# Kernel optimization log

Measured on AMD Instinct MI355X. Metric: run time of the kernel, lower is better.

## Reference

```python
import jax, jax.numpy as jnp
import numpy as np
from jax.ops import segment_sum

N_NODES = 100000
N_EDGES = 1600000
N_GRAPHS = 128


def setup_inputs() -> dict:
    key = jax.random.key(0)
    ks = jax.random.split(key, 16)
    x = jax.random.normal(ks[0], (N_NODES, 128), dtype=jnp.float32)
    edge_index = jax.random.randint(ks[1], (2, N_EDGES), 0, N_NODES, dtype=jnp.int64)
    batch = jnp.sort(jax.random.randint(ks[2], (N_NODES,), 0, N_GRAPHS, dtype=jnp.int64))
    def glorot(k, fan_in, fan_out):
        lim = (6.0 / (fan_in + fan_out)) ** 0.5
        return jax.random.uniform(k, (fan_in, fan_out), jnp.float32, -lim, lim)
    return {
        "x": x, "edge_index": edge_index, "batch": batch,
        "W1": glorot(ks[3], 128, 64), "b1": jnp.zeros((64,), jnp.float32),
        "W2": glorot(ks[4], 64, 64),  "b2": jnp.zeros((64,), jnp.float32),
        "W3": glorot(ks[5], 64, 64),  "b3": jnp.zeros((64,), jnp.float32),
        "W4": glorot(ks[6], 64, 64),  "b4": jnp.zeros((64,), jnp.float32),
        "Wl": glorot(ks[7], 64, 1),   "bl": jnp.zeros((1,), jnp.float32),
    }


def _gcn_layer(x, row, col, norm, W, b):
    # x: [N, Cin] -> [N, Cout]; gather source feats, scale, scatter-add at target
    h = x @ W                                 # dense transform first (GCNConv order)
    msg = norm[:, None] * h[row]              # [E, Cout]
    out = segment_sum(msg, col, num_segments=N_NODES)
    return out + b


def reference(x, edge_index, batch, W1, b1, W2, b2, W3, b3, W4, b4, Wl, bl):
    row, col = edge_index[0], edge_index[1]
    # symmetric degree normalization based on in-degree of col (PyG degree(col))
    deg = segment_sum(jnp.ones((N_EDGES,), x.dtype), col, num_segments=N_NODES)
    dinv = jnp.where(deg > 0, deg ** -0.5, jnp.zeros_like(deg))
    norm = dinv[row] * dinv[col]              # [E]

    h = _gcn_layer(x, row, col, norm, W1, b1)
    h = _gcn_layer(h, row, col, norm, W2, b2)
    h = _gcn_layer(h, row, col, norm, W3, b3)
    h = _gcn_layer(h, row, col, norm, W4, b4)  # [N, 64]

    # to_dense_batch + mean(dim=1): padded zeros count, so divide by max graph size
    sums = segment_sum(h, batch, num_segments=N_GRAPHS)          # [B, 64]
    counts = segment_sum(jnp.ones((N_NODES,), h.dtype), batch, num_segments=N_GRAPHS)
    n_max = jnp.max(counts)
    pooled = sums / n_max                                        # [B, 64]
    return pooled @ Wl + bl                                      # [B, 1]
```

## Files before the change

### kernel.cpp

```cpp
#include <hip/hip_runtime.h>
#include <hip/hip_bf16.h>
#include <hip/hip_fp16.h>

#define N_NODES 100000
#define N_EDGES 1600000
#define N_GRAPHS 128

#define BSH 9
#define BNODES 512
#define NB 196
#define CAP 12288
#define BLK 512
#define EPB (N_EDGES / BLK)
#define RECMAX 10240

#define SPLIT 4


__global__ __launch_bounds__(256) void k_hist(const int* __restrict__ col,
                                              int* __restrict__ hist_t) {
    __shared__ int h[NB];
    const int t = threadIdx.x, b = blockIdx.x;
    for (int i = t; i < NB; i += 256) h[i] = 0;
    __syncthreads();
    const int e0 = b * EPB;
    for (int i = t; i < EPB; i += 256) atomicAdd(&h[col[e0 + i] >> BSH], 1);
    __syncthreads();
    for (int i = t; i < NB; i += 256) hist_t[i * BLK + b] = h[i];
}

__global__ __launch_bounds__(512) void k_cursors(const int* __restrict__ hist_t,
                                                 int* __restrict__ cursors,
                                                 int* __restrict__ bcnt) {
    __shared__ int s[BLK];
    const int t = threadIdx.x, bin = blockIdx.x;
    const int v = hist_t[bin * BLK + t];
    s[t] = v; __syncthreads();
    for (int off = 1; off < BLK; off <<= 1) {
        int a = (t >= off) ? s[t - off] : 0;
        __syncthreads(); s[t] += a; __syncthreads();
    }
    cursors[bin * BLK + t] = bin * CAP + s[t] - v;
    if (t == BLK - 1) bcnt[bin] = s[t];
}

__global__ __launch_bounds__(256) void k_mid(const int* __restrict__ row,
                                             const int* __restrict__ col,
                                             const int* __restrict__ cursors,
                                             int* __restrict__ bedges) {
    __shared__ int cur[NB];
    const int t = threadIdx.x, b = blockIdx.x;
    for (int i = t; i < NB; i += 256) cur[i] = cursors[i * BLK + b];
    __syncthreads();
    const int e0 = b * EPB;
    for (int i = t; i < EPB; i += 256) {
        const int c = col[e0 + i];
        const int r = row[e0 + i];
        const int pos = atomicAdd(&cur[c >> BSH], 1);
        bedges[pos] = r | ((c & (BNODES - 1)) << 17);
    }
}

__global__ __launch_bounds__(512) void k_build(const int* __restrict__ bedges,
                                               const int* __restrict__ bcnt,
                                               int* __restrict__ csr,
                                               int* __restrict__ offs,
                                               int* __restrict__ deg_c,
                                               float* __restrict__ dinv) {
    __shared__ int rec[RECMAX];
    __shared__ int deg[BNODES];
    __shared__ int offx[BNODES];
    __shared__ int cur[BNODES];
    const int t = threadIdx.x, bin = blockIdx.x;
    const int base = bin * CAP;
    const int cnt = bcnt[bin];
    const int vb = bin << BSH;
    const int nn = min(BNODES, N_NODES - vb);
    for (int i = t; i < cnt; i += 512) rec[i] = bedges[base + i];
    deg[t] = 0;
    __syncthreads();
    for (int i = t; i < cnt; i += 512) atomicAdd(&deg[(rec[i] >> 17) & (BNODES - 1)], 1);
    __syncthreads();
    const int d = (t < nn) ? deg[t] : 0;
    const int pd = (d + 7) & ~7;
    offx[t] = pd; __syncthreads();
    for (int off = 1; off < BNODES; off <<= 1) {
        int a = (t >= off) ? offx[t - off] : 0;
        __syncthreads(); offx[t] += a; __syncthreads();
    }
    const int myoff = offx[t] - pd;
    cur[t] = myoff;
    if (t < nn) {
        offs[vb + t] = base + myoff;
        deg_c[vb + t] = d;
        dinv[vb + t] = (d > 0) ? rsqrtf((float)d) : 0.0f;
        for (int j = d; j < pd; j++) csr[base + myoff + j] = N_NODES;
    }
    __syncthreads();
    for (int i = t; i < cnt; i += 512) {
        const int r = rec[i];
        const int pos = atomicAdd(&cur[(r >> 17) & (BNODES - 1)], 1);
        csr[base + pos] = r & 0x1FFFF;
    }
}


template <int CIN>
__global__ __launch_bounds__(256) void k_gemm(const float* __restrict__ X,
                                              const float* __restrict__ W,
                                              const float* __restrict__ dinv,
                                              __half* __restrict__ H16) {
    constexpr int STR = 68;
    __shared__ float sX[64 * STR];
    __shared__ float sW[64 * 64];
    const int t = threadIdx.x;
    const int nb = blockIdx.x * 64;
    const int tx = t & 15;
    const int ty = t >> 4;
    const int c0 = tx * 4, n0 = ty * 4;

    float acc[4][4] = {};

    for (int k0 = 0; k0 < CIN; k0 += 64) {
        if (k0) __syncthreads();
        for (int i = t; i < 64 * 16; i += 256) {
            const int k = i >> 4, c4 = (i & 15) * 4;
            *reinterpret_cast<float4*>(&sW[k * 64 + c4]) =
                *reinterpret_cast<const float4*>(W + (size_t)(k0 + k) * 64 + c4);
        }
        for (int i = t; i < 64 * 16; i += 256) {
            const int node = i >> 4, k4 = (i & 15) * 4;
            const int gn = nb + node;
            float4 v = make_float4(0.f, 0.f, 0.f, 0.f);
            if (gn < N_NODES)
                v = *reinterpret_cast<const float4*>(X + (size_t)gn * CIN + k0 + k4);
            *reinterpret_cast<float4*>(&sX[node * STR + k4]) = v;
        }
        __syncthreads();

        const float* xb = &sX[n0 * STR];
        #pragma unroll 4
        for (int k = 0; k < 64; k++) {
            const float4 b = *reinterpret_cast<const float4*>(&sW[k * 64 + c0]);
            const float a0 = xb[k];
            const float a1 = xb[STR + k];
            const float a2 = xb[2 * STR + k];
            const float a3 = xb[3 * STR + k];
            acc[0][0] += a0 * b.x; acc[0][1] += a0 * b.y; acc[0][2] += a0 * b.z; acc[0][3] += a0 * b.w;
            acc[1][0] += a1 * b.x; acc[1][1] += a1 * b.y; acc[1][2] += a1 * b.z; acc[1][3] += a1 * b.w;
            acc[2][0] += a2 * b.x; acc[2][1] += a2 * b.y; acc[2][2] += a2 * b.z; acc[2][3] += a2 * b.w;
            acc[3][0] += a3 * b.x; acc[3][1] += a3 * b.y; acc[3][2] += a3 * b.z; acc[3][3] += a3 * b.w;
        }
    }

    #pragma unroll
    for (int n = 0; n < 4; n++) {
        const int gn = nb + n0 + n;
        if (gn < N_NODES) {
            const float dv = dinv[gn];
            const __half2 p0 = __floats2half2_rn(acc[n][0] * dv, acc[n][1] * dv);
            const __half2 p1 = __floats2half2_rn(acc[n][2] * dv, acc[n][3] * dv);
            __half2* dst = reinterpret_cast<__half2*>(H16 + (size_t)gn * 64 + c0);
            dst[0] = p0; dst[1] = p1;
        }
    }
}


__global__ __launch_bounds__(256) void k_prop(const __half* __restrict__ Hin,
                                              const int* __restrict__ csr,
                                              const int* __restrict__ offs,
                                              const int* __restrict__ deg_c,
                                              const float* __restrict__ dinv,
                                              const float* __restrict__ bias,
                                              float* __restrict__ Hout) {
    const int wave = threadIdx.x >> 6, lane = threadIdx.x & 63;
    const int v = blockIdx.x * 4 + wave;
    if (v >= N_NODES) return;
    const int c2 = lane & 31;
    const int half = lane >> 5;
    const int start = offs[v];
    const int cntp = (deg_c[v] + 7) & ~7;
    const int* ep = csr + start;
    const __half* hb = Hin + c2 * 2;
    float ax = 0.f, ay = 0.f;
    for (int j = 0; j < cntp; j += 8) {
        const int4 q0 = *reinterpret_cast<const int4*>(ep + j);
        const int4 q1 = *reinterpret_cast<const int4*>(ep + j + 4);
        const int i0 = half ? q0.y : q0.x;
        const int i1 = half ? q0.w : q0.z;
        const int i2 = half ? q1.y : q1.x;
        const int i3 = half ? q1.w : q1.z;
        const __half2 h0 = *reinterpret_cast<const __half2*>(hb + (size_t)i0 * 64);
        const __half2 h1 = *reinterpret_cast<const __half2*>(hb + (size_t)i1 * 64);
        const __half2 h2 = *reinterpret_cast<const __half2*>(hb + (size_t)i2 * 64);
        const __half2 h3 = *reinterpret_cast<const __half2*>(hb + (size_t)i3 * 64);
        const float2 f0 = __half22float2(h0);
        const float2 f1 = __half22float2(h1);
        const float2 f2 = __half22float2(h2);
        const float2 f3 = __half22float2(h3);
        ax += (f0.x + f1.x) + (f2.x + f3.x);
        ay += (f0.y + f1.y) + (f2.y + f3.y);
    }
    ax += __shfl_xor(ax, 32, 64);
    ay += __shfl_xor(ay, 32, 64);
    if (half == 0) {
        const float dv = dinv[v];
        float2 o;
        o.x = dv * ax + bias[c2 * 2];
        o.y = dv * ay + bias[c2 * 2 + 1];
        *reinterpret_cast<float2*>(Hout + (size_t)v * 64 + c2 * 2) = o;
    }
}


__global__ __launch_bounds__(256) void k_pool(const float* __restrict__ H,
                                              const int* __restrict__ batch,
                                              float* __restrict__ partial) {
    const int g = blockIdx.x >> 2;
    const int s = blockIdx.x & (SPLIT - 1);
    int lo = 0, hi = N_NODES;
    while (lo < hi) { int m = (lo + hi) >> 1; if (batch[m] < g) lo = m + 1; else hi = m; }
    const int a = lo;
    lo = 0; hi = N_NODES;
    while (lo < hi) { int m = (lo + hi) >> 1; if (batch[m] < g + 1) lo = m + 1; else hi = m; }
    const int b = lo;

    const int wave = threadIdx.x >> 6, lane = threadIdx.x & 63;
    const int lane16 = s * 4 + wave;
    float ac0 = 0.f, ac1 = 0.f, ac2 = 0.f, ac3 = 0.f;
    int v = a + lane16;
    for (; v + 48 < b; v += 64) {
        ac0 += H[(size_t)v * 64 + lane];
        ac1 += H[(size_t)(v + 16) * 64 + lane];
        ac2 += H[(size_t)(v + 32) * 64 + lane];
        ac3 += H[(size_t)(v + 48) * 64 + lane];
    }
    for (; v < b; v += 16) ac0 += H[(size_t)v * 64 + lane];
    const float acc = (ac0 + ac1) + (ac2 + ac3);

    __shared__ float red[4][64];
    red[wave][lane] = acc;
    __syncthreads();
    if (wave == 0) {
        const float r = (red[0][lane] + red[1][lane]) + (red[2][lane] + red[3][lane]);
        partial[((size_t)s * N_GRAPHS + g) * 64 + lane] = r;
    }
}

__global__ void k_final(const float* __restrict__ partial, const int* __restrict__ batch,
                        const float* __restrict__ Wl, const float* __restrict__ bl,
                        float* __restrict__ out) {
    __shared__ int scnt[128];
    int t = threadIdx.x;
    int lo = 0, hi = N_NODES;
    while (lo < hi) { int mid = (lo + hi) >> 1; if (batch[mid] < t) lo = mid + 1; else hi = mid; }
    int a = lo;
    lo = 0; hi = N_NODES;
    while (lo < hi) { int mid = (lo + hi) >> 1; if (batch[mid] < t + 1) lo = mid + 1; else hi = mid; }
    scnt[t] = lo - a;
    __syncthreads();
    for (int off = 64; off > 0; off >>= 1) {
        if (t < off) scnt[t] = max(scnt[t], scnt[t + off]);
        __syncthreads();
    }
    const float nmax = (float)scnt[0];
    float s = 0.f;
    for (int c = 0; c < 64; c++) {
        float g = 0.f;
        #pragma unroll
        for (int p = 0; p < SPLIT; p++)
            g += partial[((size_t)p * N_GRAPHS + t) * 64 + c];
        s += g * Wl[c];
    }
    out[t] = s / nmax + bl[0];
}


extern "C" void kernel_launch(void* const* d_in, const int* in_sizes, int n_in,
                              void* d_out, int out_size, void* d_ws, size_t ws_size,
                              hipStream_t stream) {
    const float* x    = (const float*)d_in[0];
    const int*   ei   = (const int*)d_in[1];
    const int*   batch= (const int*)d_in[2];
    const float* W1 = (const float*)d_in[3];  const float* b1 = (const float*)d_in[4];
    const float* W2 = (const float*)d_in[5];  const float* b2 = (const float*)d_in[6];
    const float* W3 = (const float*)d_in[7];  const float* b3 = (const float*)d_in[8];
    const float* W4 = (const float*)d_in[9];  const float* b4 = (const float*)d_in[10];
    const float* Wl = (const float*)d_in[11]; const float* bl = (const float*)d_in[12];
    float* out = (float*)d_out;

    const int* row = ei;
    const int* col = ei + N_EDGES;

    char* ws = (char*)d_ws;
    size_t off = 0;
    auto alloc = [&](size_t bytes) {
        void* p = ws + off;
        off = (off + bytes + 255) & ~(size_t)255;
        return p;
    };
    int*    hist_t  = (int*)alloc((size_t)NB * BLK * 4);
    int*    cursors = (int*)alloc((size_t)NB * BLK * 4);
    int*    bcnt    = (int*)alloc(NB * 4);
    int*    bedges  = (int*)alloc((size_t)NB * CAP * 4);
    int*    csr     = bedges;
    int*    offs    = (int*)alloc(N_NODES * 4);
    int*    deg_c   = (int*)alloc(N_NODES * 4);
    float*  dinv    = (float*)alloc(N_NODES * 4);
    __half* h16     = (__half*)alloc((size_t)(N_NODES + 1) * 64 * 2);
    float*  h_b     = (float*)alloc((size_t)N_NODES * 64 * 4);
    float*  partial = (float*)alloc((size_t)SPLIT * N_GRAPHS * 64 * 4);

    hipMemsetAsync(h16 + (size_t)N_NODES * 64, 0, 64 * 2, stream);

    k_hist<<<BLK, 256, 0, stream>>>(col, hist_t);
    k_cursors<<<NB, 512, 0, stream>>>(hist_t, cursors, bcnt);
    k_mid<<<BLK, 256, 0, stream>>>(row, col, cursors, bedges);
    k_build<<<NB, 512, 0, stream>>>(bedges, bcnt, csr, offs, deg_c, dinv);

    const int GB = (N_NODES + 63) / 64;

    k_gemm<128><<<GB, 256, 0, stream>>>(x, W1, dinv, h16);
    k_prop<<<N_NODES / 4, 256, 0, stream>>>(h16, csr, offs, deg_c, dinv, b1, h_b);
    k_gemm<64><<<GB, 256, 0, stream>>>(h_b, W2, dinv, h16);
    k_prop<<<N_NODES / 4, 256, 0, stream>>>(h16, csr, offs, deg_c, dinv, b2, h_b);
    k_gemm<64><<<GB, 256, 0, stream>>>(h_b, W3, dinv, h16);
    k_prop<<<N_NODES / 4, 256, 0, stream>>>(h16, csr, offs, deg_c, dinv, b3, h_b);
    k_gemm<64><<<GB, 256, 0, stream>>>(h_b, W4, dinv, h16);
    k_prop<<<N_NODES / 4, 256, 0, stream>>>(h16, csr, offs, deg_c, dinv, b4, h_b);

    k_pool<<<N_GRAPHS * SPLIT, 256, 0, stream>>>(h_b, batch, partial);
    k_final<<<1, 128, 0, stream>>>(partial, batch, Wl, bl, out);
}
```

Before: 447.1 us.

## Pad CSR rows to 4 and widen GEMM tile to 128 nodes

CSR rows are now padded to a multiple of 4 instead of 8, so the propagation kernel performs fewer wasted sentinel gathers. Its loop now consumes 4 edges per iteration instead of 8. The GEMM kernel now covers 128 nodes per block, with each thread computing 4 nodes by 8 columns and writing 16-byte half stores. This improves register-level reuse of the shared-memory loads. The trade-offs are fewer independent gathers in flight per iteration in propagation, and higher register and LDS use per block in the GEMM.

```diff
diff --git a/kernel.cpp b/kernel.cpp
--- a/kernel.cpp
+++ b/kernel.cpp
@@ -82,7 +82,7 @@
     for (int i = t; i < cnt; i += 512) atomicAdd(&deg[(rec[i] >> 17) & (BNODES - 1)], 1);
     __syncthreads();
     const int d = (t < nn) ? deg[t] : 0;
-    const int pd = (d + 7) & ~7;
+    const int pd = (d + 3) & ~3;
     offx[t] = pd; __syncthreads();
     for (int off = 1; off < BNODES; off <<= 1) {
         int a = (t >= off) ? offx[t - off] : 0;
@@ -110,16 +110,16 @@
                                               const float* __restrict__ W,
                                               const float* __restrict__ dinv,
                                               __half* __restrict__ H16) {
-    constexpr int STR = 68;
-    __shared__ float sX[64 * STR];
+    constexpr int STR = 66;
+    __shared__ float sX[128 * STR];
     __shared__ float sW[64 * 64];
     const int t = threadIdx.x;
-    const int nb = blockIdx.x * 64;
-    const int tx = t & 15;
-    const int ty = t >> 4;
-    const int c0 = tx * 4, n0 = ty * 4;
-
-    float acc[4][4] = {};
+    const int nb = blockIdx.x * 128;
+    const int tx = t & 7;
+    const int ty = t >> 3;
+    const int c0 = tx * 8, n0 = ty * 4;
+
+    float acc[4][8] = {};
 
     for (int k0 = 0; k0 < CIN; k0 += 64) {
         if (k0) __syncthreads();
@@ -128,28 +128,35 @@
             *reinterpret_cast<float4*>(&sW[k * 64 + c4]) =
                 *reinterpret_cast<const float4*>(W + (size_t)(k0 + k) * 64 + c4);
         }
-        for (int i = t; i < 64 * 16; i += 256) {
+        for (int i = t; i < 128 * 16; i += 256) {
             const int node = i >> 4, k4 = (i & 15) * 4;
             const int gn = nb + node;
             float4 v = make_float4(0.f, 0.f, 0.f, 0.f);
             if (gn < N_NODES)
                 v = *reinterpret_cast<const float4*>(X + (size_t)gn * CIN + k0 + k4);
-            *reinterpret_cast<float4*>(&sX[node * STR + k4]) = v;
+            float* dst = &sX[node * STR + k4];
+            *reinterpret_cast<float2*>(dst) = make_float2(v.x, v.y);
+            *reinterpret_cast<float2*>(dst + 2) = make_float2(v.z, v.w);
         }
         __syncthreads();
 
         const float* xb = &sX[n0 * STR];
         #pragma unroll 4
         for (int k = 0; k < 64; k++) {
-            const float4 b = *reinterpret_cast<const float4*>(&sW[k * 64 + c0]);
+            const float4 b0 = *reinterpret_cast<const float4*>(&sW[k * 64 + c0]);
+            const float4 b1 = *reinterpret_cast<const float4*>(&sW[k * 64 + c0 + 4]);
             const float a0 = xb[k];
             const float a1 = xb[STR + k];
             const float a2 = xb[2 * STR + k];
             const float a3 = xb[3 * STR + k];
-            acc[0][0] += a0 * b.x; acc[0][1] += a0 * b.y; acc[0][2] += a0 * b.z; acc[0][3] += a0 * b.w;
-            acc[1][0] += a1 * b.x; acc[1][1] += a1 * b.y; acc[1][2] += a1 * b.z; acc[1][3] += a1 * b.w;
-            acc[2][0] += a2 * b.x; acc[2][1] += a2 * b.y; acc[2][2] += a2 * b.z; acc[2][3] += a2 * b.w;
-            acc[3][0] += a3 * b.x; acc[3][1] += a3 * b.y; acc[3][2] += a3 * b.z; acc[3][3] += a3 * b.w;
+            acc[0][0] += a0 * b0.x; acc[0][1] += a0 * b0.y; acc[0][2] += a0 * b0.z; acc[0][3] += a0 * b0.w;
+            acc[0][4] += a0 * b1.x; acc[0][5] += a0 * b1.y; acc[0][6] += a0 * b1.z; acc[0][7] += a0 * b1.w;
+            acc[1][0] += a1 * b0.x; acc[1][1] += a1 * b0.y; acc[1][2] += a1 * b0.z; acc[1][3] += a1 * b0.w;
+            acc[1][4] += a1 * b1.x; acc[1][5] += a1 * b1.y; acc[1][6] += a1 * b1.z; acc[1][7] += a1 * b1.w;
+            acc[2][0] += a2 * b0.x; acc[2][1] += a2 * b0.y; acc[2][2] += a2 * b0.z; acc[2][3] += a2 * b0.w;
+            acc[2][4] += a2 * b1.x; acc[2][5] += a2 * b1.y; acc[2][6] += a2 * b1.z; acc[2][7] += a2 * b1.w;
+            acc[3][0] += a3 * b0.x; acc[3][1] += a3 * b0.y; acc[3][2] += a3 * b0.z; acc[3][3] += a3 * b0.w;
+            acc[3][4] += a3 * b1.x; acc[3][5] += a3 * b1.y; acc[3][6] += a3 * b1.z; acc[3][7] += a3 * b1.w;
         }
     }
 
@@ -158,10 +165,12 @@
         const int gn = nb + n0 + n;
         if (gn < N_NODES) {
             const float dv = dinv[gn];
-            const __half2 p0 = __floats2half2_rn(acc[n][0] * dv, acc[n][1] * dv);
-            const __half2 p1 = __floats2half2_rn(acc[n][2] * dv, acc[n][3] * dv);
-            __half2* dst = reinterpret_cast<__half2*>(H16 + (size_t)gn * 64 + c0);
-            dst[0] = p0; dst[1] = p1;
+            __half2 h[4];
+            #pragma unroll
+            for (int q = 0; q < 4; q++)
+                h[q] = __floats2half2_rn(acc[n][2 * q] * dv, acc[n][2 * q + 1] * dv);
+            *reinterpret_cast<int4*>(H16 + (size_t)gn * 64 + c0) =
+                *reinterpret_cast<const int4*>(h);
         }
     }
 }
@@ -180,27 +189,20 @@
     const int c2 = lane & 31;
     const int half = lane >> 5;
     const int start = offs[v];
-    const int cntp = (deg_c[v] + 7) & ~7;
+    const int cntp = (deg_c[v] + 3) & ~3;
     const int* ep = csr + start;
     const __half* hb = Hin + c2 * 2;
     float ax = 0.f, ay = 0.f;
-    for (int j = 0; j < cntp; j += 8) {
-        const int4 q0 = *reinterpret_cast<const int4*>(ep + j);
-        const int4 q1 = *reinterpret_cast<const int4*>(ep + j + 4);
-        const int i0 = half ? q0.y : q0.x;
-        const int i1 = half ? q0.w : q0.z;
-        const int i2 = half ? q1.y : q1.x;
-        const int i3 = half ? q1.w : q1.z;
+    for (int j = 0; j < cntp; j += 4) {
+        const int4 q = *reinterpret_cast<const int4*>(ep + j);
+        const int i0 = half ? q.y : q.x;
+        const int i1 = half ? q.w : q.z;
         const __half2 h0 = *reinterpret_cast<const __half2*>(hb + (size_t)i0 * 64);
         const __half2 h1 = *reinterpret_cast<const __half2*>(hb + (size_t)i1 * 64);
-        const __half2 h2 = *reinterpret_cast<const __half2*>(hb + (size_t)i2 * 64);
-        const __half2 h3 = *reinterpret_cast<const __half2*>(hb + (size_t)i3 * 64);
         const float2 f0 = __half22float2(h0);
         const float2 f1 = __half22float2(h1);
-        const float2 f2 = __half22float2(h2);
-        const float2 f3 = __half22float2(h3);
-        ax += (f0.x + f1.x) + (f2.x + f3.x);
-        ay += (f0.y + f1.y) + (f2.y + f3.y);
+        ax += f0.x + f1.x;
+        ay += f0.y + f1.y;
     }
     ax += __shfl_xor(ax, 32, 64);
     ay += __shfl_xor(ay, 32, 64);
@@ -319,7 +321,7 @@
     k_mid<<<BLK, 256, 0, stream>>>(row, col, cursors, bedges);
     k_build<<<NB, 512, 0, stream>>>(bedges, bcnt, csr, offs, deg_c, dinv);
 
-    const int GB = (N_NODES + 63) / 64;
+    const int GB = (N_NODES + 127) / 128;
 
     k_gemm<128><<<GB, 256, 0, stream>>>(x, W1, dinv, h16);
     k_prop<<<N_NODES / 4, 256, 0, stream>>>(h16, csr, offs, deg_c, dinv, b1, h_b);
```

After: 508.5 us. +13.7%, slower.
